# Kernel tuning notes

Measured on AMD Instinct MI355X. Metric: run time of the kernel, lower is better.

Reference implementation:

```python
import jax, jax.numpy as jnp
import numpy as np

D, S, E, MPE = 256, 128, 512, 4096
B, N = 2, 4096


def _rope(x):
    # x: (..., n, d); RoPE over axis -2 positions (dim=1 in the torch code)
    n, d = x.shape[-2], x.shape[-1]
    half = d // 2
    pos = jnp.arange(n, dtype=x.dtype)
    inv_freq = 10000.0 ** (-jnp.arange(half, dtype=x.dtype) / half)
    sinusoid = pos[:, None] * inv_freq  # (n, half)
    sin, cos = jnp.sin(sinusoid), jnp.cos(sinusoid)
    x1, x2 = jnp.split(x, 2, axis=-1)
    return jnp.concatenate([x1 * cos - x2 * sin, x2 * cos + x1 * sin], axis=-1)


def setup_inputs() -> dict:
    key = jax.random.key(0)
    ks = jax.random.split(key, 12)
    std = 0.02
    return {
        "query": jax.random.normal(ks[0], (B, N, D), jnp.float32),
        "ln_w": jnp.ones((D,), jnp.float32),
        "ln_b": jnp.zeros((D,), jnp.float32),
        "Wu": jax.random.normal(ks[1], (D, E), jnp.float32) / np.float32(np.sqrt(D)),
        "bu": jnp.zeros((E,), jnp.float32),
        "Wv": jax.random.normal(ks[2], (D, E), jnp.float32) / np.float32(np.sqrt(D)),
        "bv": jnp.zeros((E,), jnp.float32),
        "Wbase": jax.random.normal(ks[3], (D, S), jnp.float32) / np.float32(np.sqrt(D)),
        "bbase": jnp.zeros((S,), jnp.float32),
        "q_w": jax.random.normal(ks[4], (1, S), jnp.float32) * std,
        "q_b": jnp.zeros((1, S), jnp.float32),
        "k_w": jax.random.normal(ks[5], (1, S), jnp.float32) * std,
        "k_b": jnp.zeros((1, S), jnp.float32),
        "w_rel": jax.random.normal(ks[6], (2 * MPE - 1,), jnp.float32) * std,
        "Wo": jax.random.normal(ks[7], (E, D), jnp.float32) / np.float32(np.sqrt(E)),
        "bo": jnp.zeros((D,), jnp.float32),
    }


def reference(query, ln_w, ln_b, Wu, bu, Wv, bv, Wbase, bbase,
              q_w, q_b, k_w, k_b, w_rel, Wo, bo):
    mpe = (w_rel.shape[0] + 1) // 2
    bsz, n, d = query.shape
    # LayerNorm
    mu = query.mean(axis=-1, keepdims=True)
    var = ((query - mu) ** 2).mean(axis=-1, keepdims=True)
    x = (query - mu) * jax.lax.rsqrt(var + 1e-5) * ln_w + ln_b
    # gated projections
    u = jax.nn.silu(x @ Wu + bu)       # (B,N,E)
    v = jax.nn.silu(x @ Wv + bv)       # (B,N,E)
    base = jax.nn.silu(x @ Wbase + bbase)  # (B,N,S)
    q = _rope(base * q_w + q_b)
    k = _rope(base * k_w + k_b)
    qk = jnp.einsum('bms,bns->bmn', q, k)  # (B,N,N)
    # Toeplitz relative-position bias: bias[i,j] = w_rel[mpe-1 + j - i]
    # (equivalent to the torch pad/repeat/reshape construction, sliced to n)
    i = jnp.arange(n)
    bias = w_rel[(mpe - 1) + i[None, :] - i[:, None]]  # (N,N)
    kernel = jnp.square(jax.nn.relu(qk / mpe + bias))
    out = (u * jnp.einsum('bmn,bne->bme', kernel, v)) @ Wo + bo
    return out
```

## Files before the change

kernel.cpp:

```cpp
#include <hip/hip_runtime.h>
#include <hip/hip_bf16.h>
#include <math.h>

typedef __bf16 bf16_8 __attribute__((ext_vector_type(8)));
typedef float f32x4 __attribute__((ext_vector_type(4)));
typedef float f32x16 __attribute__((ext_vector_type(16)));

#define D_ 256
#define S_ 128
#define E_ 512
#define MPE_ 4096
#define B_ 2
#define N_ 4096
#define M_TOT (B_*N_)

__device__ __forceinline__ ushort f2b(float f) {
  union { float f; uint u; } x; x.f = f;
  uint r = (x.u + 0x7FFFu + ((x.u >> 16) & 1u)) >> 16;
  return (ushort)r;
}
__device__ __forceinline__ float b2f(ushort b) {
  union { uint u; float f; } x; x.u = ((uint)b) << 16;
  return x.f;
}

__device__ __forceinline__ void gl_lds16(const void* g, void* l) {
  __builtin_amdgcn_global_load_lds(
      (const __attribute__((address_space(1))) void*)g,
      (__attribute__((address_space(3))) void*)l, 16, 0, 0);
}

__global__ __launch_bounds__(256) void ln_kernel(const float* __restrict__ q,
    const float* __restrict__ w, const float* __restrict__ b,
    ushort* __restrict__ x) {
  int wid = threadIdx.x >> 6, lane = threadIdx.x & 63;
  int row = blockIdx.x * 4 + wid;
  const float* qr = q + (size_t)row * D_;
  float4 v = *(const float4*)(qr + lane * 4);
  float s  = v.x + v.y + v.z + v.w;
  float ss = v.x*v.x + v.y*v.y + v.z*v.z + v.w*v.w;
  #pragma unroll
  for (int off = 32; off; off >>= 1) {
    s  += __shfl_xor(s, off);
    ss += __shfl_xor(ss, off);
  }
  float mu   = s * (1.0f / 256.0f);
  float var  = ss * (1.0f / 256.0f) - mu * mu;
  float rstd = rsqrtf(var + 1e-5f);
  ushort4 o;
  float vv[4] = {v.x, v.y, v.z, v.w};
  ushort ot[4];
  #pragma unroll
  for (int j = 0; j < 4; ++j) {
    int c = lane * 4 + j;
    ot[j] = f2b((vv[j] - mu) * rstd * w[c] + b[c]);
  }
  o.x = ot[0]; o.y = ot[1]; o.z = ot[2]; o.w = ot[3];
  *(ushort4*)(x + (size_t)row * D_ + lane * 4) = o;
}

__global__ __launch_bounds__(256) void prep_kernel(
    const float* __restrict__ Wu, const float* __restrict__ Wv,
    const float* __restrict__ Wb, const float* __restrict__ Wo,
    const float* __restrict__ w_rel,
    ushort* __restrict__ WUT, ushort* __restrict__ WVT,
    ushort* __restrict__ WBT, ushort* __restrict__ WOT,
    float* __restrict__ wrep) {
  int blk = blockIdx.x, tid = threadIdx.x;
  if (blk < 512) {
    int o = blk * 256 + tid; int c = o >> 8, r = o & 255;
    WUT[o] = f2b(Wu[r * 512 + c]);
  } else if (blk < 1024) {
    int o = (blk - 512) * 256 + tid; int c = o >> 8, r = o & 255;
    WVT[o] = f2b(Wv[r * 512 + c]);
  } else if (blk < 1152) {
    int o = (blk - 1024) * 256 + tid; int c = o >> 8, r = o & 255;
    WBT[o] = f2b(Wb[r * 128 + c]);
  } else if (blk < 1664) {
    int o = (blk - 1152) * 256 + tid; int c = o >> 9, r = o & 511;
    WOT[o] = f2b(Wo[r * 256 + c]);
  } else {
    int idx = (blk - 1664) * 256 + tid;
    int c = idx >> 13, i = idx & 8191;
    int s = i + c; if (s > 8190) s = 8190;
    wrep[idx] = w_rel[s];
  }
}

template<int EPI>
__global__ __launch_bounds__(256) void gemm_kernel(
    const ushort* __restrict__ A, const ushort* __restrict__ Bt,
    const float* __restrict__ bias, void* __restrict__ out,
    int M, int N, int K) {
  __shared__ alignas(16) ushort As[128 * 64];
  __shared__ alignas(16) ushort Bs[64 * 64];
  int tid = threadIdx.x;
  int lane = tid & 63, wid = tid >> 6;
  int m0 = blockIdx.x * 128, n0 = blockIdx.y * 64;
  int r16 = lane & 15, kq = lane >> 4;
  f32x4 acc[2][4] = {};
  for (int k0 = 0; k0 < K; k0 += 64) {
    __syncthreads();
    #pragma unroll
    for (int t = 0; t < 4; ++t) {
      int cid = tid + t * 256;
      int row = cid >> 3, c = cid & 7;
      uint4 d = *(const uint4*)(A + ((size_t)(m0 + row) * K + k0 + c * 8));
      *(uint4*)&As[row * 64 + ((c ^ (row & 7)) * 8)] = d;
    }
    #pragma unroll
    for (int t = 0; t < 2; ++t) {
      int cid = tid + t * 256;
      int row = cid >> 3, c = cid & 7;
      uint4 d = *(const uint4*)(Bt + ((size_t)(n0 + row) * K + k0 + c * 8));
      *(uint4*)&Bs[row * 64 + ((c ^ (row & 7)) * 8)] = d;
    }
    __syncthreads();
    #pragma unroll
    for (int ks = 0; ks < 2; ++ks) {
      bf16_8 af[2], bfr[4];
      int c = ks * 4 + kq;
      #pragma unroll
      for (int fm = 0; fm < 2; ++fm) {
        int r = wid * 32 + fm * 16 + r16;
        af[fm] = *(const bf16_8*)&As[r * 64 + ((c ^ (r & 7)) * 8)];
      }
      #pragma unroll
      for (int fn = 0; fn < 4; ++fn) {
        int r = fn * 16 + r16;
        bfr[fn] = *(const bf16_8*)&Bs[r * 64 + ((c ^ (r & 7)) * 8)];
      }
      #pragma unroll
      for (int fm = 0; fm < 2; ++fm)
        #pragma unroll
        for (int fn = 0; fn < 4; ++fn)
          acc[fm][fn] = __builtin_amdgcn_mfma_f32_16x16x32_bf16(af[fm], bfr[fn], acc[fm][fn], 0, 0, 0);
    }
  }
  #pragma unroll
  for (int fm = 0; fm < 2; ++fm)
    #pragma unroll
    for (int fn = 0; fn < 4; ++fn)
      #pragma unroll
      for (int reg = 0; reg < 4; ++reg) {
        int ml = wid * 32 + fm * 16 + kq * 4 + reg;
        int nl = fn * 16 + r16;
        size_t gm = m0 + ml, gn = n0 + nl;
        float val = acc[fm][fn][reg] + bias[gn];
        if (EPI == 0) {
          float y = val / (1.0f + expf(-val));
          ((ushort*)out)[gm * N + gn] = f2b(y);
        } else if (EPI == 2) {
          float y = val / (1.0f + expf(-val));
          int bb = (int)(gm >> 12), n = (int)(gm & 4095);
          int t = n >> 6, nn = n & 63;
          int nh = nn >> 5, nl2 = nn & 31;
          int kb2 = nl2 >> 4, hi = (nl2 >> 3) & 1, j = nl2 & 7;
          int eb = (int)(gn >> 5), l31e = (int)(gn & 31);
          size_t addr = ((((size_t)(bb * 64 + t) * 2 + nh) * 2 + kb2) * 16 + eb) * 512
                      + (hi * 32 + l31e) * 8 + j;
          ((ushort*)out)[addr] = f2b(y);
        } else {
          ((float*)out)[gm * N + gn] = val;
        }
      }
}

__global__ __launch_bounds__(256) void rope_kernel(const ushort* __restrict__ base,
    const float* __restrict__ qw, const float* __restrict__ qb,
    const float* __restrict__ kw, const float* __restrict__ kb_,
    ushort* __restrict__ Q, ushort* __restrict__ KF) {
  int g = blockIdx.x * 256 + threadIdx.x;
  int row = g >> 6, i = g & 63;
  int n = row & (N_ - 1);
  float invf = powf(10000.0f, -(float)i * (1.0f / 64.0f));
  float sv, cv;
  sincosf((float)n * invf, &sv, &cv);
  const float sc = 0.015625f;
  float b1 = b2f(base[row * S_ + i]), b2 = b2f(base[row * S_ + 64 + i]);
  float x1q = b1 * qw[i] + qb[i], x2q = b2 * qw[64 + i] + qb[64 + i];
  Q[row * S_ + i]      = f2b((x1q * cv - x2q * sv) * sc);
  Q[row * S_ + 64 + i] = f2b((x2q * cv + x1q * sv) * sc);
  float x1k = b1 * kw[i] + kb_[i], x2k = b2 * kw[64 + i] + kb_[64 + i];
  float k1 = (x1k * cv - x2k * sv) * sc;
  float k2 = (x2k * cv + x1k * sv) * sc;
  int bb = row >> 12, t = n >> 6, nn = n & 63;
  int nh = nn >> 5, l31 = nn & 31;
  int kb1 = i >> 4, hi1 = (i >> 3) & 1, j1 = i & 7;
  size_t fb = (size_t)((bb * 64 + t) * 2 + nh) * 8;
  KF[(fb + kb1) * 512 + (hi1 * 32 + l31) * 8 + j1] = f2b(k1);
  KF[(fb + 4 + kb1) * 512 + (hi1 * 32 + l31) * 8 + j1] = f2b(k2);
}

__global__ __launch_bounds__(512, 2) void attn_kernel(
    const ushort* __restrict__ Q, const ushort* __restrict__ KF,
    const ushort* __restrict__ VF, const ushort* __restrict__ U,
    const float* __restrict__ wrep, ushort* __restrict__ KVU) {
  __shared__ alignas(16) ushort SMEM_[65536];
  const int tid = threadIdx.x, lane = tid & 63, wid = tid >> 6;
  const int wg = wid >> 1, nh = wid & 1;
  const int b = blockIdx.z, m0 = blockIdx.x * 128, e0 = blockIdx.y * 128;
  const int l31 = lane & 31, hi = lane >> 5;
  const int mrow = m0 + wg * 32 + l31;

  const int bbase = 4095 + nh * 32 + 4 * hi - mrow;
  const int csel = bbase & 3;
  const float* wrow = wrep + csel * 8192 + (bbase - csel);

  bf16_8 qf[8];
  #pragma unroll
  for (int kb = 0; kb < 8; ++kb)
    qf[kb] = *(const bf16_8*)(Q + ((size_t)(b * N_ + mrow) * S_ + kb * 16 + hi * 8));

  auto stage_kv = [&](int bi, int t) {
    const ushort* ksrc = KF + (size_t)(b * 64 + t) * 8192;
    #pragma unroll
    for (int tt = 0; tt < 2; ++tt) {
      int cb = tt * 8 + wid;
      gl_lds16(ksrc + cb * 512 + lane * 8, SMEM_ + bi * 8192 + cb * 512);
    }
    #pragma unroll
    for (int tt = 0; tt < 2; ++tt) {
      int f = tt * 8 + wid;
      int nh2 = f >> 3, kb2 = (f >> 2) & 1, ebl = f & 3;
      size_t fragidx = (((size_t)(b * 64 + t) * 2 + nh2) * 2 + kb2) * 16 + (e0 >> 5) + ebl;
      gl_lds16(VF + fragidx * 512 + lane * 8, SMEM_ + 32768 + bi * 8192 + f * 512);
    }
  };

  f32x16 acc[4] = {};
  uint4 paA[2], paB[2];

  auto do_pv = [&](int vb, const uint4 (&paR)[2]) {
    const ushort* vsb = SMEM_ + 32768 + vb * 8192;
    __builtin_amdgcn_s_setprio(1);
    #pragma unroll
    for (int kb = 0; kb < 2; ++kb) {
      bf16_8 pa = *(const bf16_8*)&paR[kb];
      #pragma unroll
      for (int et = 0; et < 4; ++et) {
        bf16_8 vf = *(const bf16_8*)(vsb + (nh * 8 + kb * 4 + et) * 512 + lane * 8);
        acc[et] = __builtin_amdgcn_mfma_f32_32x32x16_bf16(pa, vf, acc[et], 0, 0, 0);
      }
    }
    __builtin_amdgcn_s_setprio(0);
  };

  auto body = [&](int t, int CUR, int PRV, int NXT, uint4 (&paW)[2],
                  const uint4 (&paR)[2], bool doPV, bool doStage) {
    float4 b4[4];
    #pragma unroll
    for (int rg = 0; rg < 4; ++rg)
      b4[rg] = *(const float4*)(wrow + 64 * t + 8 * rg);
    __builtin_amdgcn_sched_barrier(0);
    if (doStage) stage_kv(NXT, t + 2);
    __builtin_amdgcn_sched_barrier(0);
    const ushort* ksb = SMEM_ + CUR * 8192;
    f32x16 s0;
    #pragma unroll
    for (int rg = 0; rg < 4; ++rg) {
      s0[4*rg+0] = b4[rg].x; s0[4*rg+1] = b4[rg].y;
      s0[4*rg+2] = b4[rg].z; s0[4*rg+3] = b4[rg].w;
    }
    __builtin_amdgcn_s_setprio(1);
    #pragma unroll
    for (int kb = 0; kb < 8; ++kb) {
      bf16_8 kf = *(const bf16_8*)(ksb + (nh * 8 + kb) * 512 + lane * 8);
      s0 = __builtin_amdgcn_mfma_f32_32x32x16_bf16(kf, qf[kb], s0, 0, 0, 0);
    }
    __builtin_amdgcn_s_setprio(0);
    if (doPV) do_pv(PRV, paR);
    uint w0[4], w1[4];
    #pragma unroll
    for (int rg = 0; rg < 4; ++rg) {
      float t0 = fmaxf(s0[4*rg+0], 0.f); t0 *= t0;
      float t1 = fmaxf(s0[4*rg+1], 0.f); t1 *= t1;
      float t2 = fmaxf(s0[4*rg+2], 0.f); t2 *= t2;
      float t3 = fmaxf(s0[4*rg+3], 0.f); t3 *= t3;
      asm("v_cvt_pk_bf16_f32 %0, %1, %2" : "=v"(w0[rg]) : "v"(t0), "v"(t1));
      asm("v_cvt_pk_bf16_f32 %0, %1, %2" : "=v"(w1[rg]) : "v"(t2), "v"(t3));
    }
    #pragma unroll
    for (int kb = 0; kb < 2; ++kb) {
      int rs = 2 * kb;
      uint x0 = w0[rs], y0 = w0[rs + 1];
      asm("v_permlane32_swap_b32 %0, %1" : "+v"(x0), "+v"(y0));
      uint x1 = w1[rs], y1 = w1[rs + 1];
      asm("v_permlane32_swap_b32 %0, %1" : "+v"(x1), "+v"(y1));
      uint4 pk; pk.x = x0; pk.y = x1; pk.z = y0; pk.w = y1;
      paW[kb] = pk;
    }
    asm volatile("s_waitcnt vmcnt(4)" ::: "memory");
    __builtin_amdgcn_s_barrier();
  };

  stage_kv(0, 0);
  stage_kv(1, 1);
  asm volatile("s_waitcnt vmcnt(4)" ::: "memory");
  __builtin_amdgcn_s_barrier();

  for (int u = 0; u < 16; ++u) {
    int t0i = 4 * u;
    body(t0i,     0, 3, 2, paA, paB, t0i > 0, t0i     <= 61);
    body(t0i + 1, 1, 0, 3, paB, paA, true,    t0i + 1 <= 61);
    body(t0i + 2, 2, 1, 0, paA, paB, true,    t0i + 2 <= 61);
    body(t0i + 3, 3, 2, 1, paB, paA, true,    t0i + 3 <= 61);
  }
  asm volatile("s_waitcnt vmcnt(0)" ::: "memory");
  do_pv(3, paB);

  __syncthreads();
  float* red = (float*)SMEM_;
  if (nh == 1) {
    #pragma unroll
    for (int et = 0; et < 4; ++et)
      #pragma unroll
      for (int rg4 = 0; rg4 < 4; ++rg4) {
        float4 w;
        w.x = acc[et][4*rg4+0]; w.y = acc[et][4*rg4+1];
        w.z = acc[et][4*rg4+2]; w.w = acc[et][4*rg4+3];
        *(float4*)&red[wg * 4096 + et * 1024 + rg4 * 256 + lane * 4] = w;
      }
  }
  __syncthreads();
  if (nh == 0) {
    #pragma unroll
    for (int et = 0; et < 4; ++et)
      #pragma unroll
      for (int rg4 = 0; rg4 < 4; ++rg4) {
        float4 r = *(const float4*)&red[wg * 4096 + et * 1024 + rg4 * 256 + lane * 4];
        acc[et][4*rg4+0] += r.x; acc[et][4*rg4+1] += r.y;
        acc[et][4*rg4+2] += r.z; acc[et][4*rg4+3] += r.w;
      }
    #pragma unroll
    for (int et = 0; et < 4; ++et)
      #pragma unroll
      for (int reg = 0; reg < 16; ++reg) {
        int ml = (reg & 3) + 8 * (reg >> 2) + 4 * hi;
        size_t grow = (size_t)b * N_ + m0 + wg * 32 + ml;
        size_t ge = e0 + et * 32 + l31;
        float uu = b2f(U[grow * E_ + ge]);
        KVU[grow * E_ + ge] = f2b(uu * acc[et][reg]);
      }
  }
}

extern "C" void kernel_launch(void* const* d_in, const int* in_sizes, int n_in,
                              void* d_out, int out_size, void* d_ws, size_t ws_size,
                              hipStream_t stream) {
  const float* query = (const float*)d_in[0];
  const float* ln_w  = (const float*)d_in[1];
  const float* ln_b  = (const float*)d_in[2];
  const float* Wu    = (const float*)d_in[3];
  const float* bu    = (const float*)d_in[4];
  const float* Wv    = (const float*)d_in[5];
  const float* bv    = (const float*)d_in[6];
  const float* Wbase = (const float*)d_in[7];
  const float* bbase = (const float*)d_in[8];
  const float* q_w   = (const float*)d_in[9];
  const float* q_b   = (const float*)d_in[10];
  const float* k_w   = (const float*)d_in[11];
  const float* k_b   = (const float*)d_in[12];
  const float* w_rel = (const float*)d_in[13];
  const float* Wo    = (const float*)d_in[14];
  const float* bo    = (const float*)d_in[15];
  float* out = (float*)d_out;

  char* ws = (char*)d_ws;
  ushort* X    = (ushort*)(ws);
  ushort* U    = (ushort*)(ws + (4u  << 20));
  ushort* VF   = (ushort*)(ws + (12u << 20));
  ushort* BASE = (ushort*)(ws + (20u << 20));
  ushort* Qb   = (ushort*)(ws + (22u << 20));
  ushort* KF   = (ushort*)(ws + (24u << 20));
  ushort* KVU  = (ushort*)(ws + (26u << 20));
  ushort* WUT  = (ushort*)(ws + (34u << 20));
  ushort* WVT  = (ushort*)(ws + (34u << 20) + 512*256*2);
  ushort* WBT  = (ushort*)(ws + (34u << 20) + 2*512*256*2);
  ushort* WOT  = (ushort*)(ws + (34u << 20) + 2*512*256*2 + 128*256*2);
  float*  WREP = (float*)(ws + (35u << 20));

  ln_kernel<<<2048, 256, 0, stream>>>(query, ln_w, ln_b, X);
  prep_kernel<<<1792, 256, 0, stream>>>(Wu, Wv, Wbase, Wo, w_rel,
                                        WUT, WVT, WBT, WOT, WREP);
  gemm_kernel<0><<<dim3(64, 8), 256, 0, stream>>>(X, WUT, bu, U, 8192, 512, 256);
  gemm_kernel<2><<<dim3(64, 8), 256, 0, stream>>>(X, WVT, bv, VF, 8192, 512, 256);
  gemm_kernel<0><<<dim3(64, 2), 256, 0, stream>>>(X, WBT, bbase, BASE, 8192, 128, 256);
  rope_kernel<<<2048, 256, 0, stream>>>(BASE, q_w, q_b, k_w, k_b, Qb, KF);
  attn_kernel<<<dim3(32, 4, 2), 512, 0, stream>>>(Qb, KF, VF, U, WREP, KVU);
  gemm_kernel<1><<<dim3(64, 4), 256, 0, stream>>>(KVU, WOT, bo, out, 8192, 256, 512);
}
```

Before: 166.2 us.

## Halve attention E-tile to 64 and restructure K/V staging for higher occupancy

The attention kernel now covers 64 E columns per block instead of 128, which doubles the grid and halves the PV accumulators. The launch bound is raised to 4 blocks per CU, and LDS shrinks to 56KB. K staging changes from four buffers to two, and V uses a 3-buffer ring, both prefetched one tile ahead with a new waitcnt and a re-unrolled loop. The aim is more waves per CU to hide latency, at the cost of recomputing QK^T and the bias twice as often across E blocks, and of a shallower prefetch.

```diff
diff --git a/kernel.cpp b/kernel.cpp
--- a/kernel.cpp
+++ b/kernel.cpp
@@ -192,14 +192,14 @@
   KF[(fb + 4 + kb1) * 512 + (hi1 * 32 + l31) * 8 + j1] = f2b(k2);
 }
 
-__global__ __launch_bounds__(512, 2) void attn_kernel(
+__global__ __launch_bounds__(512, 4) void attn_kernel(
     const ushort* __restrict__ Q, const ushort* __restrict__ KF,
     const ushort* __restrict__ VF, const ushort* __restrict__ U,
     const float* __restrict__ wrep, ushort* __restrict__ KVU) {
-  __shared__ alignas(16) ushort SMEM_[65536];
+  __shared__ alignas(16) char SMEM_[57344];
   const int tid = threadIdx.x, lane = tid & 63, wid = tid >> 6;
   const int wg = wid >> 1, nh = wid & 1;
-  const int b = blockIdx.z, m0 = blockIdx.x * 128, e0 = blockIdx.y * 128;
+  const int b = blockIdx.z, m0 = blockIdx.x * 128, e0 = blockIdx.y * 64;
   const int l31 = lane & 31, hi = lane >> 5;
   const int mrow = m0 + wg * 32 + l31;
 
@@ -212,50 +212,49 @@
   for (int kb = 0; kb < 8; ++kb)
     qf[kb] = *(const bf16_8*)(Q + ((size_t)(b * N_ + mrow) * S_ + kb * 16 + hi * 8));
 
-  auto stage_kv = [&](int bi, int t) {
+  auto stage_k = [&](int kc, int t) {
     const ushort* ksrc = KF + (size_t)(b * 64 + t) * 8192;
     #pragma unroll
     for (int tt = 0; tt < 2; ++tt) {
       int cb = tt * 8 + wid;
-      gl_lds16(ksrc + cb * 512 + lane * 8, SMEM_ + bi * 8192 + cb * 512);
-    }
-    #pragma unroll
-    for (int tt = 0; tt < 2; ++tt) {
-      int f = tt * 8 + wid;
-      int nh2 = f >> 3, kb2 = (f >> 2) & 1, ebl = f & 3;
-      size_t fragidx = (((size_t)(b * 64 + t) * 2 + nh2) * 2 + kb2) * 16 + (e0 >> 5) + ebl;
-      gl_lds16(VF + fragidx * 512 + lane * 8, SMEM_ + 32768 + bi * 8192 + f * 512);
+      gl_lds16(ksrc + cb * 512 + lane * 8, SMEM_ + kc * 16384 + cb * 1024 + lane * 16);
     }
   };
-
-  f32x16 acc[4] = {};
+  auto stage_v = [&](int vb, int t) {
+    int nh2 = wid >> 2, kb2 = (wid >> 1) & 1, ebl = wid & 1;
+    size_t fragidx = (((size_t)(b * 64 + t) * 2 + nh2) * 2 + kb2) * 16 + (e0 >> 5) + ebl;
+    gl_lds16(VF + fragidx * 512 + lane * 8,
+             SMEM_ + 32768 + vb * 8192 + wid * 1024 + lane * 16);
+  };
+
+  f32x16 acc[2] = {};
   uint4 paA[2], paB[2];
 
   auto do_pv = [&](int vb, const uint4 (&paR)[2]) {
-    const ushort* vsb = SMEM_ + 32768 + vb * 8192;
+    const char* vsb = SMEM_ + 32768 + vb * 8192;
     __builtin_amdgcn_s_setprio(1);
     #pragma unroll
     for (int kb = 0; kb < 2; ++kb) {
       bf16_8 pa = *(const bf16_8*)&paR[kb];
       #pragma unroll
-      for (int et = 0; et < 4; ++et) {
-        bf16_8 vf = *(const bf16_8*)(vsb + (nh * 8 + kb * 4 + et) * 512 + lane * 8);
+      for (int et = 0; et < 2; ++et) {
+        bf16_8 vf = *(const bf16_8*)(vsb + (nh * 4 + kb * 2 + et) * 1024 + lane * 16);
         acc[et] = __builtin_amdgcn_mfma_f32_32x32x16_bf16(pa, vf, acc[et], 0, 0, 0);
       }
     }
     __builtin_amdgcn_s_setprio(0);
   };
 
-  auto body = [&](int t, int CUR, int PRV, int NXT, uint4 (&paW)[2],
+  auto body = [&](int t, int kc, int vw, int vr, uint4 (&paW)[2],
                   const uint4 (&paR)[2], bool doPV, bool doStage) {
     float4 b4[4];
     #pragma unroll
     for (int rg = 0; rg < 4; ++rg)
       b4[rg] = *(const float4*)(wrow + 64 * t + 8 * rg);
     __builtin_amdgcn_sched_barrier(0);
-    if (doStage) stage_kv(NXT, t + 2);
+    if (doStage) { stage_k(kc ^ 1, t + 1); stage_v(vw, t + 1); }
     __builtin_amdgcn_sched_barrier(0);
-    const ushort* ksb = SMEM_ + CUR * 8192;
+    const char* ksb = SMEM_ + kc * 16384;
     f32x16 s0;
     #pragma unroll
     for (int rg = 0; rg < 4; ++rg) {
@@ -265,11 +264,11 @@
     __builtin_amdgcn_s_setprio(1);
     #pragma unroll
     for (int kb = 0; kb < 8; ++kb) {
-      bf16_8 kf = *(const bf16_8*)(ksb + (nh * 8 + kb) * 512 + lane * 8);
+      bf16_8 kf = *(const bf16_8*)(ksb + (nh * 8 + kb) * 1024 + lane * 16);
       s0 = __builtin_amdgcn_mfma_f32_32x32x16_bf16(kf, qf[kb], s0, 0, 0, 0);
     }
     __builtin_amdgcn_s_setprio(0);
-    if (doPV) do_pv(PRV, paR);
+    if (doPV) do_pv(vr, paR);
     uint w0[4], w1[4];
     #pragma unroll
     for (int rg = 0; rg < 4; ++rg) {
@@ -290,50 +289,56 @@
       uint4 pk; pk.x = x0; pk.y = x1; pk.z = y0; pk.w = y1;
       paW[kb] = pk;
     }
-    asm volatile("s_waitcnt vmcnt(4)" ::: "memory");
+    asm volatile("s_waitcnt vmcnt(1)" ::: "memory");
     __builtin_amdgcn_s_barrier();
   };
 
-  stage_kv(0, 0);
-  stage_kv(1, 1);
-  asm volatile("s_waitcnt vmcnt(4)" ::: "memory");
+  stage_k(0, 0);
+  stage_v(0, 0);
+  asm volatile("s_waitcnt vmcnt(0)" ::: "memory");
   __builtin_amdgcn_s_barrier();
 
-  for (int u = 0; u < 16; ++u) {
-    int t0i = 4 * u;
-    body(t0i,     0, 3, 2, paA, paB, t0i > 0, t0i     <= 61);
-    body(t0i + 1, 1, 0, 3, paB, paA, true,    t0i + 1 <= 61);
-    body(t0i + 2, 2, 1, 0, paA, paB, true,    t0i + 2 <= 61);
-    body(t0i + 3, 3, 2, 1, paB, paA, true,    t0i + 3 <= 61);
-  }
+  body(0, 0, 1, 0, paA, paB, false, true);
+  for (int u = 0; u < 10; ++u) {
+    int t0i = 6 * u;
+    body(t0i + 1, 1, 2, 0, paB, paA, true, true);
+    body(t0i + 2, 0, 0, 1, paA, paB, true, true);
+    body(t0i + 3, 1, 1, 2, paB, paA, true, true);
+    body(t0i + 4, 0, 2, 0, paA, paB, true, true);
+    body(t0i + 5, 1, 0, 1, paB, paA, true, true);
+    body(t0i + 6, 0, 1, 2, paA, paB, true, true);
+  }
+  body(61, 1, 2, 0, paB, paA, true, true);
+  body(62, 0, 0, 1, paA, paB, true, true);
+  body(63, 1, 0, 2, paB, paA, true, false);
   asm volatile("s_waitcnt vmcnt(0)" ::: "memory");
-  do_pv(3, paB);
+  do_pv(0, paB);
 
   __syncthreads();
   float* red = (float*)SMEM_;
   if (nh == 1) {
     #pragma unroll
-    for (int et = 0; et < 4; ++et)
+    for (int et = 0; et < 2; ++et)
       #pragma unroll
       for (int rg4 = 0; rg4 < 4; ++rg4) {
         float4 w;
         w.x = acc[et][4*rg4+0]; w.y = acc[et][4*rg4+1];
         w.z = acc[et][4*rg4+2]; w.w = acc[et][4*rg4+3];
-        *(float4*)&red[wg * 4096 + et * 1024 + rg4 * 256 + lane * 4] = w;
+        *(float4*)&red[wg * 2048 + et * 1024 + rg4 * 256 + lane * 4] = w;
       }
   }
   __syncthreads();
   if (nh == 0) {
     #pragma unroll
-    for (int et = 0; et < 4; ++et)
+    for (int et = 0; et < 2; ++et)
       #pragma unroll
       for (int rg4 = 0; rg4 < 4; ++rg4) {
-        float4 r = *(const float4*)&red[wg * 4096 + et * 1024 + rg4 * 256 + lane * 4];
+        float4 r = *(const float4*)&red[wg * 2048 + et * 1024 + rg4 * 256 + lane * 4];
         acc[et][4*rg4+0] += r.x; acc[et][4*rg4+1] += r.y;
         acc[et][4*rg4+2] += r.z; acc[et][4*rg4+3] += r.w;
       }
     #pragma unroll
-    for (int et = 0; et < 4; ++et)
+    for (int et = 0; et < 2; ++et)
       #pragma unroll
       for (int reg = 0; reg < 16; ++reg) {
         int ml = (reg & 3) + 8 * (reg >> 2) + 4 * hi;
@@ -387,6 +392,6 @@
   gemm_kernel<2><<<dim3(64, 8), 256, 0, stream>>>(X, WVT, bv, VF, 8192, 512, 256);
   gemm_kernel<0><<<dim3(64, 2), 256, 0, stream>>>(X, WBT, bbase, BASE, 8192, 128, 256);
   rope_kernel<<<2048, 256, 0, stream>>>(BASE, q_w, q_b, k_w, k_b, Qb, KF);
-  attn_kernel<<<dim3(32, 4, 2), 512, 0, stream>>>(Qb, KF, VF, U, WREP, KVU);
+  attn_kernel<<<dim3(32, 8, 2), 512, 0, stream>>>(Qb, KF, VF, U, WREP, KVU);
   gemm_kernel<1><<<dim3(64, 4), 256, 0, stream>>>(KVU, WOT, bo, out, 8192, 256, 512);
 }
```

Result: slower. 198.4 us (+19.4%).
